# Kernel tuning notes

Hardware: AMD Instinct MI355X
Metric: run time of the kernel (lower is better)

Reference implementation:

```python
import jax, jax.numpy as jnp
import numpy as np

NUM_HEADS = 16
MAX_ITERATIONS = 4
EPSILON = 3.0
MOMENTUM = 0.2
ENTROPY_PENALTY = 0.05


def setup_inputs() -> dict:
    key = jax.random.key(0)
    ks = jax.random.split(key, 6)
    B, S, D = 2, 1024, 1024
    scale = 0.02
    return {
        "x": jax.random.normal(ks[0], (B, S, D), dtype=jnp.float32),
        "wq": jax.random.normal(ks[1], (D, D), dtype=jnp.float32) * scale,
        "bq": jnp.zeros((D,), dtype=jnp.float32),
        "wk": jax.random.normal(ks[2], (D, D), dtype=jnp.float32) * scale,
        "bk": jnp.zeros((D,), dtype=jnp.float32),
        "wv": jax.random.normal(ks[3], (D, D), dtype=jnp.float32) * scale,
        "bv": jnp.zeros((D,), dtype=jnp.float32),
        "wo": jax.random.normal(ks[4], (D, D), dtype=jnp.float32) * scale,
        "bo": jnp.zeros((D,), dtype=jnp.float32),
        "res_bias": jnp.zeros((1, NUM_HEADS, 1, 1), dtype=jnp.float32),
    }


def _entropy(attn):
    # attn: [B, H, S, S] -> [B, H]; matches compute_entropy (chunking is math-neutral)
    p = attn + 1e-10
    return (-jnp.sum(p * jnp.log(p), axis=-1)).mean(axis=-1)


def reference(x, wq, bq, wk, bk, wv, bv, wo, bo, res_bias):
    B, S, D = x.shape
    H = NUM_HEADS
    hd = D // H
    # projections (torch Linear: y = x @ W^T + b)
    q = (x @ wq.T + bq).reshape(B, S, H, hd).transpose(0, 2, 1, 3)
    k = (x @ wk.T + bk).reshape(B, S, H, hd).transpose(0, 2, 1, 3)
    v = (x @ wv.T + bv).reshape(B, S, H, hd).transpose(0, 2, 1, 3)

    # scores are loop-invariant in the source (q, k never change inside the loop)
    scores = jnp.einsum("bhqd,bhkd->bhqk", q, k) / jnp.float32(hd) ** 0.5
    scores = scores + res_bias
    cur = jax.nn.softmax(scores, axis=-1)  # [B, H, S, S]

    # iteration 0
    attn = cur
    prev_attn = jax.lax.stop_gradient(attn)
    ent = _entropy(attn)                       # [B, H]
    prev_ent = jax.lax.stop_gradient(ent)
    iters = jnp.array(1, dtype=jnp.int32)
    done = jnp.all(ent.mean(axis=1) < EPSILON)  # scalar bool (torch breaks on .all())

    for t in range(1, MAX_ITERATIONS):
        blended = (1.0 - MOMENTUM) * cur + MOMENTUM * prev_attn
        new_attn = blended / blended.sum(axis=-1, keepdims=True)
        attn = jnp.where(done, attn, new_attn)
        prev_attn = jax.lax.stop_gradient(attn)

        new_ent = _entropy(attn)
        # entropy-increase penalty (per batch element)
        inc = new_ent.mean(axis=1) > prev_ent.mean(axis=1)  # [B]
        new_ent = jnp.where(inc[:, None],
                            new_ent * (1.0 - ENTROPY_PENALTY) + prev_ent * ENTROPY_PENALTY,
                            new_ent)
        ent = jnp.where(done, ent, new_ent)
        prev_ent = jax.lax.stop_gradient(ent)

        iters = jnp.where(done, iters, jnp.int32(t + 1))
        done = done | jnp.all(ent.mean(axis=1) < EPSILON)

    # output is recomputed each torch iteration but only the last survives
    attn_out = jnp.einsum("bhqk,bhkd->bhqd", attn, v)
    attn_out = attn_out.transpose(0, 2, 1, 3).reshape(B, S, D)
    out = attn_out @ wo.T + bo
    return (out, ent, iters)
```

## Files before the change

kernel.cpp:

```cpp
#include <hip/hip_runtime.h>
#include <hip/hip_bf16.h>

typedef __attribute__((ext_vector_type(4))) float f32x4;
typedef __attribute__((ext_vector_type(8))) __bf16 bf16x8;
typedef __attribute__((ext_vector_type(8))) unsigned short ushort8;

__device__ __forceinline__ unsigned short f2bf(float f) {
    unsigned u = __builtin_bit_cast(unsigned, f);
    unsigned lsb = (u >> 16) & 1u;
    u += 0x7fffu + lsb;
    return (unsigned short)(u >> 16);
}

__device__ __forceinline__ f32x4 mfma16(ushort8 a, ushort8 b, f32x4 c) {
    return __builtin_amdgcn_mfma_f32_16x16x32_bf16(
        __builtin_bit_cast(bf16x8, a), __builtin_bit_cast(bf16x8, b), c, 0, 0, 0);
}

__device__ __forceinline__ void gload_lds16(const unsigned short* g, unsigned short* l) {
    __builtin_amdgcn_global_load_lds(
        (const __attribute__((address_space(1))) unsigned int*)g,
        (__attribute__((address_space(3))) unsigned int*)l, 16, 0, 0);
}

__global__ __launch_bounds__(256) void cvt_all_kernel(
    const float* __restrict__ x, const float* __restrict__ wq, const float* __restrict__ wk,
    const float* __restrict__ wv, const float* __restrict__ wo, unsigned short* __restrict__ dst) {
    int i = blockIdx.x * blockDim.x + threadIdx.x;
    const float* src;
    size_t off;
    if (i < 262144) { src = x; off = i; }
    else {
        int j = i - 262144;
        int w = j >> 17;
        off = (size_t)(j & 131071);
        src = (w == 0) ? wq : (w == 1) ? wk : (w == 2) ? wv : wo;
    }
    float4 a = ((const float4*)src)[off * 2];
    float4 b = ((const float4*)src)[off * 2 + 1];
    ushort8 o;
    o[0] = f2bf(a.x); o[1] = f2bf(a.y); o[2] = f2bf(a.z); o[3] = f2bf(a.w);
    o[4] = f2bf(b.x); o[5] = f2bf(b.y); o[6] = f2bf(b.z); o[7] = f2bf(b.w);
    *(ushort8*)&dst[(size_t)i * 8] = o;
}

__global__ __launch_bounds__(256) void gemm_qkv(
    const unsigned short* __restrict__ xb,
    const unsigned short* __restrict__ wqb, const unsigned short* __restrict__ wkb,
    const unsigned short* __restrict__ wvb,
    const float* __restrict__ bq, const float* __restrict__ bk, const float* __restrict__ bv,
    unsigned short* __restrict__ qo, unsigned short* __restrict__ ko, unsigned short* __restrict__ vt) {
    const int N = 1024, K = 1024;
    int flat = blockIdx.x + 16 * blockIdx.y + 256 * blockIdx.z;
    int vid = (flat & 7) * 96 + (flat >> 3);
    int bx = vid & 15, by = (vid >> 4) & 15, bz = vid >> 8;
    const unsigned short* Bt = (bz == 0) ? wqb : (bz == 1) ? wkb : wvb;
    const float* bias = (bz == 0) ? bq : (bz == 1) ? bk : bv;

    __shared__ unsigned short As[2][128 * 64];
    __shared__ unsigned short Bs[2][64 * 64];
    int tid = threadIdx.x;
    int wave = tid >> 6, lane = tid & 63;
    int lr = lane & 15, lk = lane >> 4;
    int m0 = bx * 128, n0 = by * 64;
    int wr = wave >> 1, wc = wave & 1;

    f32x4 acc[4][2] = {};

    auto stage = [&](int p, int kk) {
#pragma unroll
        for (int i = 0; i < 4; ++i) {
            int c = tid + 256 * i;
            int r = c >> 3, s = c & 7;
            gload_lds16(xb + (size_t)(m0 + r) * K + kk + (s ^ (r & 7)) * 8, &As[p][c * 8]);
        }
#pragma unroll
        for (int i = 0; i < 2; ++i) {
            int c = tid + 256 * i;
            int r = c >> 3, s = c & 7;
            gload_lds16(Bt + (size_t)(n0 + r) * K + kk + (s ^ (r & 7)) * 8, &Bs[p][c * 8]);
        }
    };

    stage(0, 0);
    asm volatile("s_waitcnt vmcnt(0)" ::: "memory");
    __syncthreads();

    for (int t = 0; t < 16; ++t) {
        int p = t & 1;
        if (t < 15) stage(p ^ 1, (t + 1) * 64);
#pragma unroll
        for (int ks = 0; ks < 2; ++ks) {
            ushort8 af[4], bfr[2];
#pragma unroll
            for (int f = 0; f < 4; ++f) {
                int row = wr * 64 + f * 16 + lr;
                int cc = ks * 4 + lk;
                af[f] = *(const ushort8*)&As[p][row * 64 + ((cc ^ (row & 7)) * 8)];
            }
#pragma unroll
            for (int f = 0; f < 2; ++f) {
                int row = wc * 32 + f * 16 + lr;
                int cc = ks * 4 + lk;
                bfr[f] = *(const ushort8*)&Bs[p][row * 64 + ((cc ^ (row & 7)) * 8)];
            }
#pragma unroll
            for (int i = 0; i < 4; ++i)
#pragma unroll
                for (int j = 0; j < 2; ++j)
                    acc[i][j] = mfma16(af[i], bfr[j], acc[i][j]);
        }
        __syncthreads();
    }

    if (bz < 2) {
        unsigned short* C = (bz == 0) ? qo : ko;
#pragma unroll
        for (int i = 0; i < 4; ++i)
#pragma unroll
            for (int j = 0; j < 2; ++j)
#pragma unroll
                for (int r = 0; r < 4; ++r) {
                    int row = m0 + wr * 64 + i * 16 + lk * 4 + r;
                    int col = n0 + wc * 32 + j * 16 + lr;
                    C[(size_t)row * N + col] = f2bf(acc[i][j][r] + bias[col]);
                }
    } else {
#pragma unroll
        for (int i = 0; i < 4; ++i)
#pragma unroll
            for (int j = 0; j < 2; ++j) {
                int row = m0 + wr * 64 + i * 16 + lk * 4;
                int col = n0 + wc * 32 + j * 16 + lr;
                int b = row >> 10, n = row & 1023;
                float bb = bias[col];
                ushort4 o4;
                o4.x = f2bf(acc[i][j][0] + bb);
                o4.y = f2bf(acc[i][j][1] + bb);
                o4.z = f2bf(acc[i][j][2] + bb);
                o4.w = f2bf(acc[i][j][3] + bb);
                *(ushort4*)&vt[((size_t)(b * 16 + (col >> 6)) * 64 + (col & 63)) * 1024 + n] = o4;
            }
    }
}

__global__ __launch_bounds__(256) void gemm_out(
    const unsigned short* __restrict__ Ab, const unsigned short* __restrict__ Btb,
    const float* __restrict__ bias, float* __restrict__ C,
    const float* __restrict__ ent_part, float* __restrict__ out_ent,
    float* __restrict__ out_iters) {
    const int N = 1024, K = 1024;
    int flat = blockIdx.x + 16 * blockIdx.y;
    int vid = (flat & 7) * 32 + (flat >> 3);
    int bx = vid & 15, by = vid >> 4;
    int tid = threadIdx.x;
    int wave = tid >> 6, lane = tid & 63;

    if (flat == 0 && wave == 0) {
        float s = 0.f;
        if (lane < 32) {
            for (int i = 0; i < 16; ++i) s += ent_part[lane * 16 + i];
            s *= (1.0f / 1024.0f);
            out_ent[lane] = s;
        }
        float m = s;
        m += __shfl_xor(m, 1, 64); m += __shfl_xor(m, 2, 64);
        m += __shfl_xor(m, 4, 64); m += __shfl_xor(m, 8, 64);
        float m1 = __shfl(m, 16, 64);
        if (lane == 0) {
            float e0 = m * (1.f / 16.f), e1 = m1 * (1.f / 16.f);
            out_iters[0] = (e0 < 3.0f && e1 < 3.0f) ? 1.0f : 4.0f;
        }
    }

    __shared__ unsigned short As[2][128 * 64];
    __shared__ unsigned short Bs[2][64 * 64];
    int lr = lane & 15, lk = lane >> 4;
    int m0 = bx * 128, n0 = by * 64;
    int wr = wave >> 1, wc = wave & 1;

    f32x4 acc[4][2] = {};

    auto stage = [&](int p, int kk) {
#pragma unroll
        for (int i = 0; i < 4; ++i) {
            int c = tid + 256 * i;
            int r = c >> 3, s = c & 7;
            gload_lds16(Ab + (size_t)(m0 + r) * K + kk + (s ^ (r & 7)) * 8, &As[p][c * 8]);
        }
#pragma unroll
        for (int i = 0; i < 2; ++i) {
            int c = tid + 256 * i;
            int r = c >> 3, s = c & 7;
            gload_lds16(Btb + (size_t)(n0 + r) * K + kk + (s ^ (r & 7)) * 8, &Bs[p][c * 8]);
        }
    };

    stage(0, 0);
    asm volatile("s_waitcnt vmcnt(0)" ::: "memory");
    __syncthreads();

    for (int t = 0; t < 16; ++t) {
        int p = t & 1;
        if (t < 15) stage(p ^ 1, (t + 1) * 64);
#pragma unroll
        for (int ks = 0; ks < 2; ++ks) {
            ushort8 af[4], bfr[2];
#pragma unroll
            for (int f = 0; f < 4; ++f) {
                int row = wr * 64 + f * 16 + lr;
                int cc = ks * 4 + lk;
                af[f] = *(const ushort8*)&As[p][row * 64 + ((cc ^ (row & 7)) * 8)];
            }
#pragma unroll
            for (int f = 0; f < 2; ++f) {
                int row = wc * 32 + f * 16 + lr;
                int cc = ks * 4 + lk;
                bfr[f] = *(const ushort8*)&Bs[p][row * 64 + ((cc ^ (row & 7)) * 8)];
            }
#pragma unroll
            for (int i = 0; i < 4; ++i)
#pragma unroll
                for (int j = 0; j < 2; ++j)
                    acc[i][j] = mfma16(af[i], bfr[j], acc[i][j]);
        }
        __syncthreads();
    }

#pragma unroll
    for (int i = 0; i < 4; ++i)
#pragma unroll
        for (int j = 0; j < 2; ++j)
#pragma unroll
            for (int r = 0; r < 4; ++r) {
                int row = m0 + wr * 64 + i * 16 + lk * 4 + r;
                int col = n0 + wc * 32 + j * 16 + lr;
                C[(size_t)row * N + col] = acc[i][j][r] + bias[col];
            }
}

__global__ __launch_bounds__(256) void attn_kernel(
    const unsigned short* __restrict__ qb, const unsigned short* __restrict__ kb,
    const unsigned short* __restrict__ vtb, const float* __restrict__ res_bias,
    unsigned short* __restrict__ attn_out, float* __restrict__ ent_part) {
    const int S = 1024, D = 1024;
    const float LOG2E = 1.4426950408889634f;
    const float LN2 = 0.6931471805599453f;
    int flat = blockIdx.x + 16 * blockIdx.y;
    int vid = (flat & 7) * 64 + (flat >> 3);
    int qt = vid & 15;
    int bh = vid >> 4;
    int b = bh >> 4, h = bh & 15;
    int tid = threadIdx.x;
    int wave = tid >> 6, lane = tid & 63;
    int lr = lane & 15, lk = lane >> 4;

    __shared__ unsigned short Ks[128 * 64];
    __shared__ unsigned short Vts[64 * 128];
    __shared__ unsigned short Ps[64 * 128];
    __shared__ float wpart[4];

    const float rbl = res_bias[h] * LOG2E;
    const float c1 = 0.125f * LOG2E;
    const unsigned short* qg = qb + (size_t)(b * S + qt * 64) * D + h * 64;
    const unsigned short* kg = kb + (size_t)(b * S) * D + h * 64;
    const unsigned short* vtg = vtb + (size_t)bh * 64 * 1024;

    ushort8 qf[2];
#pragma unroll
    for (int ks = 0; ks < 2; ++ks)
        qf[ks] = *(const ushort8*)(qg + (size_t)(wave * 16 + lr) * D + (ks * 4 + lk) * 8);

    ushort8 kr[4], vr[4];
#pragma unroll
    for (int i = 0; i < 4; ++i) {
        int c = tid + 256 * i;
        kr[i] = *(const ushort8*)(kg + (size_t)(c >> 3) * D + (c & 7) * 8);
        vr[i] = *(const ushort8*)(vtg + (size_t)(c >> 4) * 1024 + (c & 15) * 8);
    }

    f32x4 o[4] = {};
    float l_ = 0.f, ps_ = 0.f;

    for (int kt = 0; kt < 8; ++kt) {
        __syncthreads();
#pragma unroll
        for (int i = 0; i < 4; ++i) {
            int c = tid + 256 * i;
            int r1 = c >> 3, d1 = c & 7;
            *(ushort8*)&Ks[r1 * 64 + ((d1 ^ (r1 & 7)) * 8)] = kr[i];
            int r2 = c >> 4, d2 = c & 15;
            *(ushort8*)&Vts[r2 * 128 + ((d2 ^ (r2 & 7)) * 8)] = vr[i];
        }
        __syncthreads();

        if (kt < 7) {
#pragma unroll
            for (int i = 0; i < 4; ++i) {
                int c = tid + 256 * i;
                kr[i] = *(const ushort8*)(kg + (size_t)((kt + 1) * 128 + (c >> 3)) * D + (c & 7) * 8);
                vr[i] = *(const ushort8*)(vtg + (size_t)(c >> 4) * 1024 + (kt + 1) * 128 + (c & 15) * 8);
            }
        }

        f32x4 sf[8] = {};
        __builtin_amdgcn_s_setprio(1);
#pragma unroll
        for (int ks = 0; ks < 2; ++ks) {
#pragma unroll
            for (int fj = 0; fj < 8; ++fj) {
                ushort8 kf = *(const ushort8*)&Ks[(fj * 16 + lr) * 64 + (((ks * 4 + lk) ^ (lr & 7)) * 8)];
                sf[fj] = mfma16(kf, qf[ks], sf[fj]);
            }
        }
        __builtin_amdgcn_s_setprio(0);

        float pl = 0.f, ps = 0.f;
#pragma unroll
        for (int fj = 0; fj < 8; ++fj)
#pragma unroll
            for (int r = 0; r < 4; ++r) {
                float t = sf[fj][r] * c1 + rbl;
                float pe = __builtin_amdgcn_exp2f(t);
                pl += pe; ps = fmaf(pe, t, ps);
                sf[fj][r] = pe;
            }
        int q = wave * 16 + lr;
#pragma unroll
        for (int fj = 0; fj < 8; ++fj) {
            ushort4 pk4;
            pk4.x = f2bf(sf[fj][0]); pk4.y = f2bf(sf[fj][1]);
            pk4.z = f2bf(sf[fj][2]); pk4.w = f2bf(sf[fj][3]);
            *(ushort4*)&Ps[q * 128 + ((fj ^ (lr & 7)) << 4) + (lk << 2)] = pk4;
        }
        pl += __shfl_xor(pl, 16, 64); pl += __shfl_xor(pl, 32, 64);
        ps += __shfl_xor(ps, 16, 64); ps += __shfl_xor(ps, 32, 64);
        l_ += pl; ps_ += ps;

        asm volatile("s_waitcnt lgkmcnt(0)" ::: "memory");
        __builtin_amdgcn_sched_barrier(0);

        __builtin_amdgcn_s_setprio(1);
#pragma unroll
        for (int ks = 0; ks < 4; ++ks) {
            int ch = (ks * 2 + (lk >> 1)) ^ (lr & 7);
            ushort8 ap = *(const ushort8*)&Ps[q * 128 + (ch << 4) + ((lk & 1) << 3)];
#pragma unroll
            for (int fd = 0; fd < 4; ++fd) {
                ushort8 bv8 = *(const ushort8*)&Vts[(fd * 16 + lr) * 128 + (((ks * 4 + lk) ^ (lr & 7)) * 8)];
                o[fd] = mfma16(ap, bv8, o[fd]);
            }
        }
        __builtin_amdgcn_s_setprio(0);
    }

    float linv = 1.f / l_;
    float ent_row = __logf(l_) - LN2 * ps_ * linv;
    float linv_r[4];
#pragma unroll
    for (int r = 0; r < 4; ++r) linv_r[r] = __shfl(linv, lk * 4 + r, 64);
#pragma unroll
    for (int r = 0; r < 4; ++r) {
        int row = b * S + qt * 64 + wave * 16 + lk * 4 + r;
#pragma unroll
        for (int fd = 0; fd < 4; ++fd) {
            int col = h * 64 + fd * 16 + lr;
            attn_out[(size_t)row * D + col] = f2bf(o[fd][r] * linv_r[r]);
        }
    }
    float es = ent_row;
    es += __shfl_xor(es, 1, 64);
    es += __shfl_xor(es, 2, 64);
    es += __shfl_xor(es, 4, 64);
    es += __shfl_xor(es, 8, 64);
    if (lane == 0) wpart[wave] = es;
    __syncthreads();
    if (tid == 0) ent_part[bh * 16 + qt] = wpart[0] + wpart[1] + wpart[2] + wpart[3];
}

extern "C" void kernel_launch(void* const* d_in, const int* in_sizes, int n_in,
                              void* d_out, int out_size, void* d_ws, size_t ws_size,
                              hipStream_t stream) {
    const float* x  = (const float*)d_in[0];
    const float* wq = (const float*)d_in[1];
    const float* bq = (const float*)d_in[2];
    const float* wk = (const float*)d_in[3];
    const float* bk = (const float*)d_in[4];
    const float* wv = (const float*)d_in[5];
    const float* bv = (const float*)d_in[6];
    const float* wo = (const float*)d_in[7];
    const float* bo = (const float*)d_in[8];
    const float* rbias = (const float*)d_in[9];

    char* ws = (char*)d_ws;
    unsigned short* xb  = (unsigned short*)(ws);
    unsigned short* wqb = (unsigned short*)(ws + ((size_t)4 << 20));
    unsigned short* wkb = (unsigned short*)(ws + ((size_t)6 << 20));
    unsigned short* wvb = (unsigned short*)(ws + ((size_t)8 << 20));
    unsigned short* wob = (unsigned short*)(ws + ((size_t)10 << 20));
    unsigned short* qbf = (unsigned short*)(ws + ((size_t)12 << 20));
    unsigned short* kbf = (unsigned short*)(ws + ((size_t)16 << 20));
    unsigned short* vtb = (unsigned short*)(ws + ((size_t)20 << 20));
    unsigned short* aob = (unsigned short*)(ws + ((size_t)24 << 20));
    float* ent_part = (float*)(ws + ((size_t)28 << 20));

    float* out = (float*)d_out;
    float* out_ent = out + (size_t)2 * 1024 * 1024;
    float* out_iters = out_ent + 32;

    cvt_all_kernel<<<dim3(3072), dim3(256), 0, stream>>>(x, wq, wk, wv, wo, xb);
    gemm_qkv<<<dim3(16, 16, 3), dim3(256), 0, stream>>>(xb, wqb, wkb, wvb, bq, bk, bv, qbf, kbf, vtb);
    attn_kernel<<<dim3(16, 32), dim3(256), 0, stream>>>(qbf, kbf, vtb, rbias, aob, ent_part);
    gemm_out<<<dim3(16, 16), dim3(256), 0, stream>>>(aob, wob, bo, out, ent_part, out_ent, out_iters);
}
```

Baseline: 68.09 us.

## Process 128 query rows per attention block to reuse K/V tiles

The attention kernel now has each wave handle two 16-row query groups, so a block covers 128 queries instead of 64 and the grid shrinks to 256 blocks. Each K and V^T fragment read from shared memory feeds two MFMAs, which halves the global and shared K/V traffic per query. The entropy partial layout changes from 16 to 8 tiles per head, and gemm_out is updated to match. The cost is more registers, a larger P buffer in shared memory, and only 256 blocks, which may leave CUs underfilled and lower occupancy.

```diff
diff --git a/kernel.cpp b/kernel.cpp
--- a/kernel.cpp
+++ b/kernel.cpp
@@ -159,7 +159,7 @@
     if (flat == 0 && wave == 0) {
         float s = 0.f;
         if (lane < 32) {
-            for (int i = 0; i < 16; ++i) s += ent_part[lane * 16 + i];
+            for (int i = 0; i < 8; ++i) s += ent_part[lane * 8 + i];
             s *= (1.0f / 1024.0f);
             out_ent[lane] = s;
         }
@@ -246,10 +246,10 @@
     const int S = 1024, D = 1024;
     const float LOG2E = 1.4426950408889634f;
     const float LN2 = 0.6931471805599453f;
-    int flat = blockIdx.x + 16 * blockIdx.y;
-    int vid = (flat & 7) * 64 + (flat >> 3);
-    int qt = vid & 15;
-    int bh = vid >> 4;
+    int flat = blockIdx.x + 8 * blockIdx.y;
+    int vid = (flat & 7) * 32 + (flat >> 3);
+    int qt = vid & 7;
+    int bh = vid >> 3;
     int b = bh >> 4, h = bh & 15;
     int tid = threadIdx.x;
     int wave = tid >> 6, lane = tid & 63;
@@ -257,19 +257,21 @@
 
     __shared__ unsigned short Ks[128 * 64];
     __shared__ unsigned short Vts[64 * 128];
-    __shared__ unsigned short Ps[64 * 128];
+    __shared__ unsigned short Ps[128 * 128];
     __shared__ float wpart[4];
 
     const float rbl = res_bias[h] * LOG2E;
     const float c1 = 0.125f * LOG2E;
-    const unsigned short* qg = qb + (size_t)(b * S + qt * 64) * D + h * 64;
+    const unsigned short* qg_ = qb + (size_t)(b * S + qt * 128) * D + h * 64;
     const unsigned short* kg = kb + (size_t)(b * S) * D + h * 64;
     const unsigned short* vtg = vtb + (size_t)bh * 64 * 1024;
 
-    ushort8 qf[2];
-#pragma unroll
-    for (int ks = 0; ks < 2; ++ks)
-        qf[ks] = *(const ushort8*)(qg + (size_t)(wave * 16 + lr) * D + (ks * 4 + lk) * 8);
+    ushort8 qf[2][2];
+#pragma unroll
+    for (int qg = 0; qg < 2; ++qg)
+#pragma unroll
+        for (int ks = 0; ks < 2; ++ks)
+            qf[qg][ks] = *(const ushort8*)(qg_ + (size_t)(wave * 32 + qg * 16 + lr) * D + (ks * 4 + lk) * 8);
 
     ushort8 kr[4], vr[4];
 #pragma unroll
@@ -279,8 +281,8 @@
         vr[i] = *(const ushort8*)(vtg + (size_t)(c >> 4) * 1024 + (c & 15) * 8);
     }
 
-    f32x4 o[4] = {};
-    float l_ = 0.f, ps_ = 0.f;
+    f32x4 o0[4] = {}, o1[4] = {};
+    float l_[2] = {0.f, 0.f}, ps_[2] = {0.f, 0.f};
 
     for (int kt = 0; kt < 8; ++kt) {
         __syncthreads();
@@ -303,39 +305,44 @@
             }
         }
 
-        f32x4 sf[8] = {};
+        f32x4 sf0[8] = {}, sf1[8] = {};
         __builtin_amdgcn_s_setprio(1);
 #pragma unroll
         for (int ks = 0; ks < 2; ++ks) {
 #pragma unroll
             for (int fj = 0; fj < 8; ++fj) {
                 ushort8 kf = *(const ushort8*)&Ks[(fj * 16 + lr) * 64 + (((ks * 4 + lk) ^ (lr & 7)) * 8)];
-                sf[fj] = mfma16(kf, qf[ks], sf[fj]);
+                sf0[fj] = mfma16(kf, qf[0][ks], sf0[fj]);
+                sf1[fj] = mfma16(kf, qf[1][ks], sf1[fj]);
             }
         }
         __builtin_amdgcn_s_setprio(0);
 
-        float pl = 0.f, ps = 0.f;
-#pragma unroll
-        for (int fj = 0; fj < 8; ++fj)
-#pragma unroll
-            for (int r = 0; r < 4; ++r) {
-                float t = sf[fj][r] * c1 + rbl;
-                float pe = __builtin_amdgcn_exp2f(t);
-                pl += pe; ps = fmaf(pe, t, ps);
-                sf[fj][r] = pe;
-            }
-        int q = wave * 16 + lr;
-#pragma unroll
-        for (int fj = 0; fj < 8; ++fj) {
-            ushort4 pk4;
-            pk4.x = f2bf(sf[fj][0]); pk4.y = f2bf(sf[fj][1]);
-            pk4.z = f2bf(sf[fj][2]); pk4.w = f2bf(sf[fj][3]);
-            *(ushort4*)&Ps[q * 128 + ((fj ^ (lr & 7)) << 4) + (lk << 2)] = pk4;
-        }
-        pl += __shfl_xor(pl, 16, 64); pl += __shfl_xor(pl, 32, 64);
-        ps += __shfl_xor(ps, 16, 64); ps += __shfl_xor(ps, 32, 64);
-        l_ += pl; ps_ += ps;
+#pragma unroll
+        for (int qg = 0; qg < 2; ++qg) {
+            f32x4* sf = qg ? sf1 : sf0;
+            float pl = 0.f, ps = 0.f;
+#pragma unroll
+            for (int fj = 0; fj < 8; ++fj)
+#pragma unroll
+                for (int r = 0; r < 4; ++r) {
+                    float t = sf[fj][r] * c1 + rbl;
+                    float pe = __builtin_amdgcn_exp2f(t);
+                    pl += pe; ps = fmaf(pe, t, ps);
+                    sf[fj][r] = pe;
+                }
+            int q = wave * 32 + qg * 16 + lr;
+#pragma unroll
+            for (int fj = 0; fj < 8; ++fj) {
+                ushort4 pk4;
+                pk4.x = f2bf(sf[fj][0]); pk4.y = f2bf(sf[fj][1]);
+                pk4.z = f2bf(sf[fj][2]); pk4.w = f2bf(sf[fj][3]);
+                *(ushort4*)&Ps[q * 128 + ((fj ^ (lr & 7)) << 4) + (lk << 2)] = pk4;
+            }
+            pl += __shfl_xor(pl, 16, 64); pl += __shfl_xor(pl, 32, 64);
+            ps += __shfl_xor(ps, 16, 64); ps += __shfl_xor(ps, 32, 64);
+            l_[qg] += pl; ps_[qg] += ps;
+        }
 
         asm volatile("s_waitcnt lgkmcnt(0)" ::: "memory");
         __builtin_amdgcn_sched_barrier(0);
@@ -344,38 +351,44 @@
 #pragma unroll
         for (int ks = 0; ks < 4; ++ks) {
             int ch = (ks * 2 + (lk >> 1)) ^ (lr & 7);
-            ushort8 ap = *(const ushort8*)&Ps[q * 128 + (ch << 4) + ((lk & 1) << 3)];
+            ushort8 ap0 = *(const ushort8*)&Ps[(wave * 32 + lr) * 128 + (ch << 4) + ((lk & 1) << 3)];
+            ushort8 ap1 = *(const ushort8*)&Ps[(wave * 32 + 16 + lr) * 128 + (ch << 4) + ((lk & 1) << 3)];
 #pragma unroll
             for (int fd = 0; fd < 4; ++fd) {
                 ushort8 bv8 = *(const ushort8*)&Vts[(fd * 16 + lr) * 128 + (((ks * 4 + lk) ^ (lr & 7)) * 8)];
-                o[fd] = mfma16(ap, bv8, o[fd]);
+                o0[fd] = mfma16(ap0, bv8, o0[fd]);
+                o1[fd] = mfma16(ap1, bv8, o1[fd]);
             }
         }
         __builtin_amdgcn_s_setprio(0);
     }
 
-    float linv = 1.f / l_;
-    float ent_row = __logf(l_) - LN2 * ps_ * linv;
-    float linv_r[4];
-#pragma unroll
-    for (int r = 0; r < 4; ++r) linv_r[r] = __shfl(linv, lk * 4 + r, 64);
-#pragma unroll
-    for (int r = 0; r < 4; ++r) {
-        int row = b * S + qt * 64 + wave * 16 + lk * 4 + r;
-#pragma unroll
-        for (int fd = 0; fd < 4; ++fd) {
-            int col = h * 64 + fd * 16 + lr;
-            attn_out[(size_t)row * D + col] = f2bf(o[fd][r] * linv_r[r]);
-        }
-    }
-    float es = ent_row;
+    float es = 0.f;
+#pragma unroll
+    for (int qg = 0; qg < 2; ++qg) {
+        f32x4* o = qg ? o1 : o0;
+        float linv = 1.f / l_[qg];
+        es += __logf(l_[qg]) - LN2 * ps_[qg] * linv;
+        float linv_r[4];
+#pragma unroll
+        for (int r = 0; r < 4; ++r) linv_r[r] = __shfl(linv, lk * 4 + r, 64);
+#pragma unroll
+        for (int r = 0; r < 4; ++r) {
+            int row = b * S + qt * 128 + wave * 32 + qg * 16 + lk * 4 + r;
+#pragma unroll
+            for (int fd = 0; fd < 4; ++fd) {
+                int col = h * 64 + fd * 16 + lr;
+                attn_out[(size_t)row * D + col] = f2bf(o[fd][r] * linv_r[r]);
+            }
+        }
+    }
     es += __shfl_xor(es, 1, 64);
     es += __shfl_xor(es, 2, 64);
     es += __shfl_xor(es, 4, 64);
     es += __shfl_xor(es, 8, 64);
     if (lane == 0) wpart[wave] = es;
     __syncthreads();
-    if (tid == 0) ent_part[bh * 16 + qt] = wpart[0] + wpart[1] + wpart[2] + wpart[3];
+    if (tid == 0) ent_part[bh * 8 + qt] = wpart[0] + wpart[1] + wpart[2] + wpart[3];
 }
 
 extern "C" void kernel_launch(void* const* d_in, const int* in_sizes, int n_in,
@@ -410,6 +423,6 @@
 
     cvt_all_kernel<<<dim3(3072), dim3(256), 0, stream>>>(x, wq, wk, wv, wo, xb);
     gemm_qkv<<<dim3(16, 16, 3), dim3(256), 0, stream>>>(xb, wqb, wkb, wvb, bq, bk, bv, qbf, kbf, vtb);
-    attn_kernel<<<dim3(16, 32), dim3(256), 0, stream>>>(qbf, kbf, vtb, rbias, aob, ent_part);
+    attn_kernel<<<dim3(8, 32), dim3(256), 0, stream>>>(qbf, kbf, vtb, rbias, aob, ent_part);
     gemm_out<<<dim3(16, 16), dim3(256), 0, stream>>>(aob, wob, bo, out, ent_part, out_ent, out_iters);
 }
```

Result: no change. 69.06 us (+1.4%).
